# Kernel tuning notes

Hardware: AMD Instinct MI355X
Metric: run time of the kernel (lower is better)

Reference implementation:

```python
import jax, jax.numpy as jnp
import numpy as np

NUM_HEADS = 16
HEAD_DIM = 64  # hidden_size 1024 / 16 heads


def setup_inputs() -> dict:
    key = jax.random.key(0)
    k1, k2, k3, k4 = jax.random.split(key, 4)
    B, S, Dm = 1, 2048, 1024
    scale = 1.0 / np.sqrt(Dm)
    return {
        "hidden_states": jax.random.normal(k1, (B, S, Dm), dtype=jnp.float32),
        "Wq": jax.random.normal(k2, (Dm, Dm), dtype=jnp.float32) * scale,
        "Wk": jax.random.normal(k3, (Dm, Dm), dtype=jnp.float32) * scale,
        "Wv": jax.random.normal(k4, (Dm, Dm), dtype=jnp.float32) * scale,
    }


def reference(hidden_states, Wq, Wk, Wv):
    # hidden_states: [B, S, Dm]; Wq/Wk/Wv: [Dm, Dm] (no bias)
    B, S, Dm = hidden_states.shape
    H, D = NUM_HEADS, HEAD_DIM
    q = (hidden_states @ Wq).reshape(B, S, H, D)
    k = (hidden_states @ Wk).reshape(B, S, H, D)
    v = (hidden_states @ Wv).reshape(B, S, H, D)
    # scaled dot-product scores: [B, H, Sq, Sk]
    scores = jnp.einsum("bqhd,bkhd->bhqk", q, k) / jnp.sqrt(jnp.float32(D))
    probs = jax.nn.softmax(scores, axis=-1)
    # context: [B, Sq, H, D] -> [B, Sq, H*D]
    context = jnp.einsum("bhqk,bkhd->bqhd", probs, v).reshape(B, S, H * D)
    # module permutes scores [B, Sq, Sk, H] -> [B, H, Sq, Sk]; we built that layout directly
    return context, probs
```

## Files before the change

kernel.cpp:

```cpp
#include <hip/hip_runtime.h>
#include <cstdint>
#include <cstddef>

#define SEQ 2048
#define DMODEL 1024
#define NHEADS 16
#define HDIM 64

typedef __attribute__((ext_vector_type(8))) short short8;
typedef __attribute__((ext_vector_type(4))) float floatx4;

__device__ __forceinline__ short f2bf(float f) {
  union { float f; uint32_t u; } x; x.f = f;
  uint32_t r = (x.u + 0x7FFFu + ((x.u >> 16) & 1u)) >> 16;
  return (short)(uint16_t)r;
}

__global__ __launch_bounds__(256) void cast_bf16_kernel(const float* __restrict__ src,
                                                        short* __restrict__ dst, int n) {
  int i = blockIdx.x * 256 + threadIdx.x;
  if (i < n) dst[i] = f2bf(src[i]);
}

__global__ __launch_bounds__(256) void transpose_cast_kernel(const float* __restrict__ src,
                                                             short* __restrict__ dst) {
  __shared__ float tile[32][33];
  int tx = threadIdx.x, ty = threadIdx.y;
  int x = blockIdx.x * 32 + tx;
  int y0 = blockIdx.y * 32;
#pragma unroll
  for (int j = 0; j < 32; j += 8)
    tile[ty + j][tx] = src[(size_t)(y0 + ty + j) * DMODEL + x];
  __syncthreads();
  int xo = blockIdx.y * 32 + tx;
  int yo0 = blockIdx.x * 32;
#pragma unroll
  for (int j = 0; j < 32; j += 8)
    dst[(size_t)(yo0 + ty + j) * DMODEL + xo] = f2bf(tile[tx][ty + j]);
}

__global__ __launch_bounds__(256) void qkv_gemm_kernel(const short* __restrict__ Xb,
                                                       const short* __restrict__ Wt,
                                                       short* __restrict__ q,
                                                       short* __restrict__ k,
                                                       short* __restrict__ vT) {
  int wave = threadIdx.x >> 6;
  int lane = threadIdx.x & 63;
  int lr = lane & 15;
  int quad = lane >> 4;
  int m0 = blockIdx.y * 64 + wave * 16;
  int n0 = blockIdx.x * 64;

  const short* Arow = Xb + (size_t)(m0 + lr) * DMODEL + quad * 8;
  const short* Brow = Wt + (size_t)(n0 + lr) * DMODEL + quad * 8;

  floatx4 acc[4] = {};
  for (int kb = 0; kb < DMODEL; kb += 32) {
    short8 a = *(const short8*)(Arow + kb);
#pragma unroll
    for (int f = 0; f < 4; ++f) {
      short8 b = *(const short8*)(Brow + (size_t)f * 16 * DMODEL + kb);
      acc[f] = __builtin_amdgcn_mfma_f32_16x16x32_bf16(a, b, acc[f], 0, 0, 0);
    }
  }

#pragma unroll
  for (int f = 0; f < 4; ++f) {
    int n = n0 + f * 16 + lr;
    int which = n >> 10;
    int nn = n & 1023;
    int h = nn >> 6, d = nn & 63;
#pragma unroll
    for (int r = 0; r < 4; ++r) {
      int row = m0 + quad * 4 + r;
      short hv = f2bf(acc[f][r]);
      if (which == 0)
        q[((size_t)h * SEQ + row) * HDIM + d] = hv;
      else if (which == 1)
        k[((size_t)h * SEQ + row) * HDIM + d] = hv;
      else
        vT[((size_t)h * HDIM + d) * SEQ + row] = hv;
    }
  }
}

#define CHUNK 256
#define PSTR (CHUNK + 8)

__global__ __launch_bounds__(256) void attn_fused_kernel(const short* __restrict__ q,
                                                         const short* __restrict__ k,
                                                         const short* __restrict__ vT,
                                                         float* __restrict__ probs,
                                                         float* __restrict__ ctx) {
  __shared__ short pbuf[4][16 * PSTR];
  __shared__ float partial[4][16][64];
  __shared__ float wred[4][16];

  int h = blockIdx.y;
  int m0 = blockIdx.x * 16;
  int wave = threadIdx.x >> 6, lane = threadIdx.x & 63;
  int lr = lane & 15, quad = lane >> 4;
  int nb = wave * 512;

  const short* Q = q + ((size_t)h * SEQ + m0 + lr) * HDIM + quad * 8;
  short8 qa0 = *(const short8*)(Q);
  short8 qa1 = *(const short8*)(Q + 32);

  const short* K = k + (size_t)h * SEQ * HDIM + quad * 8;

  floatx4 s[32];
#pragma unroll
  for (int f = 0; f < 32; ++f) {
    const short* Kr = K + (size_t)(nb + f * 16 + lr) * HDIM;
    short8 b0 = *(const short8*)(Kr);
    short8 b1 = *(const short8*)(Kr + 32);
    floatx4 t = {};
    t = __builtin_amdgcn_mfma_f32_16x16x32_bf16(qa0, b0, t, 0, 0, 0);
    s[f] = __builtin_amdgcn_mfma_f32_16x16x32_bf16(qa1, b1, t, 0, 0, 0);
  }

  float mrow[4] = {-3.4e38f, -3.4e38f, -3.4e38f, -3.4e38f};
#pragma unroll
  for (int f = 0; f < 32; ++f)
#pragma unroll
    for (int r = 0; r < 4; ++r) {
      s[f][r] *= 0.125f;
      mrow[r] = fmaxf(mrow[r], s[f][r]);
    }
#pragma unroll
  for (int off = 8; off >= 1; off >>= 1)
#pragma unroll
    for (int r = 0; r < 4; ++r) mrow[r] = fmaxf(mrow[r], __shfl_xor(mrow[r], off));
  if (lr == 0)
#pragma unroll
    for (int r = 0; r < 4; ++r) wred[wave][quad * 4 + r] = mrow[r];
  __syncthreads();
#pragma unroll
  for (int r = 0; r < 4; ++r) {
    int row = quad * 4 + r;
    mrow[r] = fmaxf(fmaxf(wred[0][row], wred[1][row]), fmaxf(wred[2][row], wred[3][row]));
  }
  __syncthreads();

  float srow[4] = {0.f, 0.f, 0.f, 0.f};
#pragma unroll
  for (int f = 0; f < 32; ++f)
#pragma unroll
    for (int r = 0; r < 4; ++r) {
      float e = __expf(s[f][r] - mrow[r]);
      s[f][r] = e;
      srow[r] += e;
    }
#pragma unroll
  for (int off = 8; off >= 1; off >>= 1)
#pragma unroll
    for (int r = 0; r < 4; ++r) srow[r] += __shfl_xor(srow[r], off);
  if (lr == 0)
#pragma unroll
    for (int r = 0; r < 4; ++r) wred[wave][quad * 4 + r] = srow[r];
  __syncthreads();
  float inv[4];
#pragma unroll
  for (int r = 0; r < 4; ++r) {
    int row = quad * 4 + r;
    inv[r] = 1.0f / (wred[0][row] + wred[1][row] + wred[2][row] + wred[3][row]);
  }

  float* Pg = probs + ((size_t)h * SEQ + m0 + quad * 4) * SEQ + nb + lr;
  short* pw = pbuf[wave];
  const short* Vbase = vT + (size_t)h * HDIM * SEQ;
  floatx4 cacc[4] = {};

#pragma unroll
  for (int c = 0; c < 2; ++c) {
#pragma unroll
    for (int fi = 0; fi < 16; ++fi) {
      int f = c * 16 + fi;
#pragma unroll
      for (int r = 0; r < 4; ++r) {
        float p = s[f][r] * inv[r];
        Pg[(size_t)r * SEQ + f * 16] = p;
        pw[(quad * 4 + r) * PSTR + fi * 16 + lr] = f2bf(p);
      }
    }
    __syncthreads();
#pragma unroll
    for (int kt = 0; kt < CHUNK; kt += 32) {
      short8 a = *(const short8*)(pw + lr * PSTR + kt + quad * 8);
#pragma unroll
      for (int f = 0; f < 4; ++f) {
        short8 b = *(const short8*)(Vbase + (size_t)(f * 16 + lr) * SEQ + nb + c * CHUNK + kt + quad * 8);
        cacc[f] = __builtin_amdgcn_mfma_f32_16x16x32_bf16(a, b, cacc[f], 0, 0, 0);
      }
    }
    __syncthreads();
  }

#pragma unroll
  for (int f = 0; f < 4; ++f)
#pragma unroll
    for (int r = 0; r < 4; ++r) partial[wave][quad * 4 + r][f * 16 + lr] = cacc[f][r];
  __syncthreads();
  for (int e = threadIdx.x; e < 16 * 64; e += 256) {
    int m = e >> 6, d = e & 63;
    float v = partial[0][m][d] + partial[1][m][d] + partial[2][m][d] + partial[3][m][d];
    ctx[(size_t)(m0 + m) * DMODEL + h * HDIM + d] = v;
  }
}

extern "C" void kernel_launch(void* const* d_in, const int* in_sizes, int n_in,
                              void* d_out, int out_size, void* d_ws, size_t ws_size,
                              hipStream_t stream) {
  const float* X = (const float*)d_in[0];
  const float* Wq = (const float*)d_in[1];
  const float* Wk = (const float*)d_in[2];
  const float* Wv = (const float*)d_in[3];

  float* ctx = (float*)d_out;
  float* probs = (float*)d_out + (size_t)SEQ * DMODEL;

  short* Xb = (short*)d_ws;
  short* Wt = Xb + (size_t)SEQ * DMODEL;
  short* qb = Wt + (size_t)3 * DMODEL * DMODEL;
  short* kb = qb + (size_t)NHEADS * SEQ * HDIM;
  short* vT = kb + (size_t)NHEADS * SEQ * HDIM;

  cast_bf16_kernel<<<(SEQ * DMODEL + 255) / 256, 256, 0, stream>>>(X, Xb, SEQ * DMODEL);
  dim3 tb(32, 8), tg(32, 32);
  transpose_cast_kernel<<<tg, tb, 0, stream>>>(Wq, Wt);
  transpose_cast_kernel<<<tg, tb, 0, stream>>>(Wk, Wt + (size_t)DMODEL * DMODEL);
  transpose_cast_kernel<<<tg, tb, 0, stream>>>(Wv, Wt + (size_t)2 * DMODEL * DMODEL);

  qkv_gemm_kernel<<<dim3(48, 32), 256, 0, stream>>>(Xb, Wt, qb, kb, vT);
  attn_fused_kernel<<<dim3(SEQ / 16, NHEADS), 256, 0, stream>>>(qb, kb, vT, probs, ctx);
}
```

Measured before the change: 543.1 us.

## Tile QKV GEMM through LDS and stream probs with coalesced nontemporal stores

The QKV projection is rewritten as a 128x128 block-tiled GEMM that stages A and B tiles in LDS with global_load_lds and computes 4x4 MFMA fragments per wave. The V output uses swapped operands so its transposed stores are contiguous. In attention, the normalized probabilities are staged in fp32 per-wave LDS and written to global memory as coalesced float4 nontemporal stores instead of scattered scalar stores, and the bf16 A operand is converted from that staging buffer. This removes the block-wide syncs in the PV loop, at the cost of more LDS and extra conversion work.

```diff
diff --git a/kernel.cpp b/kernel.cpp
--- a/kernel.cpp
+++ b/kernel.cpp
@@ -14,6 +14,11 @@
   union { float f; uint32_t u; } x; x.f = f;
   uint32_t r = (x.u + 0x7FFFu + ((x.u >> 16) & 1u)) >> 16;
   return (short)(uint16_t)r;
+}
+
+__device__ __forceinline__ void gl_lds16(const short* g, short* l) {
+  __builtin_amdgcn_global_load_lds((const __attribute__((address_space(1))) void*)g,
+                                   (__attribute__((address_space(3))) void*)l, 16, 0, 0);
 }
 
 __global__ __launch_bounds__(256) void cast_bf16_kernel(const float* __restrict__ src,
@@ -44,55 +49,88 @@
                                                        short* __restrict__ q,
                                                        short* __restrict__ k,
                                                        short* __restrict__ vT) {
-  int wave = threadIdx.x >> 6;
-  int lane = threadIdx.x & 63;
-  int lr = lane & 15;
-  int quad = lane >> 4;
-  int m0 = blockIdx.y * 64 + wave * 16;
-  int n0 = blockIdx.x * 64;
-
-  const short* Arow = Xb + (size_t)(m0 + lr) * DMODEL + quad * 8;
-  const short* Brow = Wt + (size_t)(n0 + lr) * DMODEL + quad * 8;
-
-  floatx4 acc[4] = {};
+  __shared__ short Abuf[128 * 32];
+  __shared__ short Bbuf[128 * 32];
+  int tid = threadIdx.x;
+  int wave = tid >> 6, lane = tid & 63;
+  int lr = lane & 15, quad = lane >> 4;
+  int m0 = blockIdx.y * 128;
+  int n0 = blockIdx.x * 128;
+  int wr = wave >> 1, wc = wave & 1;
+
+  const short* Ag = Xb + (size_t)(m0 + (tid >> 2)) * DMODEL + (tid & 3) * 8;
+  const short* Bg = Wt + (size_t)(n0 + (tid >> 2)) * DMODEL + (tid & 3) * 8;
+  short* Al = Abuf + wave * 512;
+  short* Bl = Bbuf + wave * 512;
+
+  floatx4 acc[4][4] = {};
+  bool isV = (n0 >= 2 * DMODEL);
+
   for (int kb = 0; kb < DMODEL; kb += 32) {
-    short8 a = *(const short8*)(Arow + kb);
-#pragma unroll
-    for (int f = 0; f < 4; ++f) {
-      short8 b = *(const short8*)(Brow + (size_t)f * 16 * DMODEL + kb);
-      acc[f] = __builtin_amdgcn_mfma_f32_16x16x32_bf16(a, b, acc[f], 0, 0, 0);
-    }
-  }
-
-#pragma unroll
-  for (int f = 0; f < 4; ++f) {
-    int n = n0 + f * 16 + lr;
-    int which = n >> 10;
-    int nn = n & 1023;
-    int h = nn >> 6, d = nn & 63;
-#pragma unroll
-    for (int r = 0; r < 4; ++r) {
-      int row = m0 + quad * 4 + r;
-      short hv = f2bf(acc[f][r]);
-      if (which == 0)
-        q[((size_t)h * SEQ + row) * HDIM + d] = hv;
-      else if (which == 1)
-        k[((size_t)h * SEQ + row) * HDIM + d] = hv;
-      else
-        vT[((size_t)h * HDIM + d) * SEQ + row] = hv;
-    }
-  }
-}
-
-#define CHUNK 256
-#define PSTR (CHUNK + 8)
+    __syncthreads();
+    gl_lds16(Ag + kb, Al);
+    gl_lds16(Ag + kb + 64 * DMODEL, Al + 2048);
+    gl_lds16(Bg + kb, Bl);
+    gl_lds16(Bg + kb + 64 * DMODEL, Bl + 2048);
+    __syncthreads();
+
+    short8 a[4], b[4];
+#pragma unroll
+    for (int i = 0; i < 4; ++i) {
+      a[i] = *(const short8*)(Abuf + (wr * 64 + i * 16 + lr) * 32 + quad * 8);
+      b[i] = *(const short8*)(Bbuf + (wc * 64 + i * 16 + lr) * 32 + quad * 8);
+    }
+    if (isV) {
+#pragma unroll
+      for (int mi = 0; mi < 4; ++mi)
+#pragma unroll
+        for (int ni = 0; ni < 4; ++ni)
+          acc[mi][ni] = __builtin_amdgcn_mfma_f32_16x16x32_bf16(b[ni], a[mi], acc[mi][ni], 0, 0, 0);
+    } else {
+#pragma unroll
+      for (int mi = 0; mi < 4; ++mi)
+#pragma unroll
+        for (int ni = 0; ni < 4; ++ni)
+          acc[mi][ni] = __builtin_amdgcn_mfma_f32_16x16x32_bf16(a[mi], b[ni], acc[mi][ni], 0, 0, 0);
+    }
+  }
+
+  if (!isV) {
+    short* out = (n0 < DMODEL) ? q : k;
+    int nbase = n0 & (DMODEL - 1);
+#pragma unroll
+    for (int mi = 0; mi < 4; ++mi)
+#pragma unroll
+      for (int ni = 0; ni < 4; ++ni) {
+        int n = nbase + wc * 64 + ni * 16 + lr;
+        int hh = n >> 6, d = n & 63;
+        size_t base = ((size_t)hh * SEQ + m0 + wr * 64 + mi * 16 + quad * 4) * HDIM + d;
+#pragma unroll
+        for (int r = 0; r < 4; ++r) out[base + (size_t)r * HDIM] = f2bf(acc[mi][ni][r]);
+      }
+  } else {
+    int nbase = n0 - 2 * DMODEL;
+#pragma unroll
+    for (int mi = 0; mi < 4; ++mi) {
+      int sidx = m0 + wr * 64 + mi * 16 + lr;
+#pragma unroll
+      for (int ni = 0; ni < 4; ++ni) {
+        int n = nbase + wc * 64 + ni * 16 + quad * 4;
+#pragma unroll
+        for (int r = 0; r < 4; ++r) vT[(size_t)(n + r) * SEQ + sidx] = f2bf(acc[mi][ni][r]);
+      }
+    }
+  }
+}
+
+#define PSTRF 132
 
 __global__ __launch_bounds__(256) void attn_fused_kernel(const short* __restrict__ q,
                                                          const short* __restrict__ k,
                                                          const short* __restrict__ vT,
                                                          float* __restrict__ probs,
                                                          float* __restrict__ ctx) {
-  __shared__ short pbuf[4][16 * PSTR];
+  __shared__ float pf[4][16 * PSTRF];
   __shared__ float partial[4][16][64];
   __shared__ float wred[4][16];
 
@@ -166,34 +204,45 @@
     inv[r] = 1.0f / (wred[0][row] + wred[1][row] + wred[2][row] + wred[3][row]);
   }
 
-  float* Pg = probs + ((size_t)h * SEQ + m0 + quad * 4) * SEQ + nb + lr;
-  short* pw = pbuf[wave];
-  const short* Vbase = vT + (size_t)h * HDIM * SEQ;
+  float* pw = pf[wave];
+  const short* Vb = vT + (size_t)h * HDIM * SEQ;
   floatx4 cacc[4] = {};
-
-#pragma unroll
-  for (int c = 0; c < 2; ++c) {
-#pragma unroll
-    for (int fi = 0; fi < 16; ++fi) {
-      int f = c * 16 + fi;
-#pragma unroll
-      for (int r = 0; r < 4; ++r) {
-        float p = s[f][r] * inv[r];
-        Pg[(size_t)r * SEQ + f * 16] = p;
-        pw[(quad * 4 + r) * PSTR + fi * 16 + lr] = f2bf(p);
-      }
-    }
-    __syncthreads();
-#pragma unroll
-    for (int kt = 0; kt < CHUNK; kt += 32) {
-      short8 a = *(const short8*)(pw + lr * PSTR + kt + quad * 8);
+  int prow = lane >> 5;
+  int pchunk = lane & 31;
+
+#pragma unroll
+  for (int c = 0; c < 4; ++c) {
+#pragma unroll
+    for (int fi = 0; fi < 8; ++fi) {
+      int f = c * 8 + fi;
+#pragma unroll
+      for (int r = 0; r < 4; ++r)
+        pw[(quad * 4 + r) * PSTRF + fi * 16 + lr] = s[f][r] * inv[r];
+    }
+#pragma unroll
+    for (int i = 0; i < 8; ++i) {
+      int row = i * 2 + prow;
+      floatx4 v4 = *(const floatx4*)(pw + row * PSTRF + pchunk * 4);
+      __builtin_nontemporal_store(
+          v4, (floatx4*)(probs + ((size_t)h * SEQ + m0 + row) * SEQ + nb + c * 128 + pchunk * 4));
+    }
+#pragma unroll
+    for (int kt = 0; kt < 128; kt += 32) {
+      const float* pa = pw + lr * PSTRF + kt + quad * 8;
+      floatx4 p0 = *(const floatx4*)(pa);
+      floatx4 p1 = *(const floatx4*)(pa + 4);
+      short8 a;
+#pragma unroll
+      for (int j = 0; j < 4; ++j) {
+        a[j] = f2bf(p0[j]);
+        a[4 + j] = f2bf(p1[j]);
+      }
 #pragma unroll
       for (int f = 0; f < 4; ++f) {
-        short8 b = *(const short8*)(Vbase + (size_t)(f * 16 + lr) * SEQ + nb + c * CHUNK + kt + quad * 8);
+        short8 b = *(const short8*)(Vb + (size_t)(f * 16 + lr) * SEQ + nb + c * 128 + kt + quad * 8);
         cacc[f] = __builtin_amdgcn_mfma_f32_16x16x32_bf16(a, b, cacc[f], 0, 0, 0);
       }
     }
-    __syncthreads();
   }
 
 #pragma unroll
@@ -231,6 +280,6 @@
   transpose_cast_kernel<<<tg, tb, 0, stream>>>(Wk, Wt + (size_t)DMODEL * DMODEL);
   transpose_cast_kernel<<<tg, tb, 0, stream>>>(Wv, Wt + (size_t)2 * DMODEL * DMODEL);
 
-  qkv_gemm_kernel<<<dim3(48, 32), 256, 0, stream>>>(Xb, Wt, qb, kb, vT);
+  qkv_gemm_kernel<<<dim3(3 * DMODEL / 128, SEQ / 128), 256, 0, stream>>>(Xb, Wt, qb, kb, vT);
   attn_fused_kernel<<<dim3(SEQ / 16, NHEADS), 256, 0, stream>>>(qb, kb, vT, probs, ctx);
 }
```

Result: faster. 447.7 us (-17.6%).
